# Kernel optimization log

Measured on AMD Instinct MI355X. Metric: run time of the kernel, lower is better.

## Reference

```python
import jax, jax.numpy as jnp
import numpy as np

T, B, D = 32, 16, 128


def _evolve(xr, xi, U):
    # xr, xi: [T,B,D,D]; U: [D,D,2] -> complex U x U^H per matrix
    Ur, Ui = U[..., 0], U[..., 1]
    r = jnp.einsum('ij,tbjk->tbik', Ur, xr) - jnp.einsum('ij,tbjk->tbik', Ui, xi)
    i = jnp.einsum('ij,tbjk->tbik', Ui, xr) + jnp.einsum('ij,tbjk->tbik', Ur, xi)
    out_r = jnp.einsum('tbik,jk->tbij', r, Ur) + jnp.einsum('tbik,jk->tbij', i, Ui)
    out_i = jnp.einsum('tbik,jk->tbij', i, Ur) - jnp.einsum('tbik,jk->tbij', r, Ui)
    return out_r, out_i


def _forward(inputs_real, inputs_imag, Uq, Uk, Uv):
    qr, qi = _evolve(inputs_real, inputs_imag, Uq)
    kr, ki = _evolve(inputs_real, inputs_imag, Uk)
    vr, vi = _evolve(inputs_real, inputs_imag, Uv)
    # trace(A @ B) = sum_ij A_ij * B_ji -> distance scores [Tq, Tk, B]
    tr_r = jnp.einsum('qbij,kbji->qkb', qr, kr) - jnp.einsum('qbij,kbji->qkb', qi, ki)
    tr_i = jnp.einsum('qbij,kbji->qkb', qr, ki) + jnp.einsum('qbij,kbji->qkb', qi, kr)
    dist = jnp.sqrt(tr_r * tr_r + tr_i * tr_i)
    # original builds scores via torch.tensor(list) -> values are detached
    dist = jax.lax.stop_gradient(dist)
    # original applies softmax over the LAST dim of the [Tk, B] score matrix,
    # i.e. over the batch dim (faithful reproduction)
    S = jax.nn.softmax(dist, axis=-1)  # [Tq, Tk, B]
    # original zip(values[0], values[1], scores) iterates the (real, imag)
    # components of the value at t=0 and t=1 against score rows 0 and 1
    s0 = S[:, 0, :, None, None]  # [Tq,B,1,1]
    s1 = S[:, 1, :, None, None]
    out_r = vr[0][None] * s0 + vi[0][None] * s1  # [Tq,B,D,D]
    out_i = vr[1][None] * s0 + vi[1][None] * s1
    return out_r, out_i


def setup_inputs() -> dict:
    key = jax.random.key(0)
    k0, k1, k2, k3, k4 = jax.random.split(key, 5)
    inputs_real = jax.random.normal(k0, (T, B, D, D), dtype=jnp.float32)
    inputs_imag = jax.random.normal(k1, (T, B, D, D), dtype=jnp.float32)
    eye = jnp.stack([jnp.eye(D, dtype=jnp.float32), jnp.zeros((D, D), jnp.float32)], axis=-1)
    Uq = eye + 0.05 * jax.random.normal(k2, (D, D, 2), dtype=jnp.float32)
    Uk = eye + 0.05 * jax.random.normal(k3, (D, D, 2), dtype=jnp.float32)
    Uv = eye + 0.05 * jax.random.normal(k4, (D, D, 2), dtype=jnp.float32)
    return {"inputs_real": inputs_real, "inputs_imag": inputs_imag, "Uq": Uq, "Uk": Uk, "Uv": Uv}


def reference(inputs_real, inputs_imag, Uq, Uk, Uv):
    return _forward(inputs_real, inputs_imag, Uq, Uk, Uv)
```

## Files before the change

kernel.cpp:

```cpp
#include <hip/hip_runtime.h>
#include <math.h>

#define TT 32
#define BB 16
#define DD 128
#define MAT 16384
#define OFF_MR   0
#define OFF_MI   16384
#define OFF_YTR  32768
#define OFF_YTI  (32768 + 64*16384)
#define OFF_ZSR  (OFF_YTI + 64*16384)
#define OFF_ZSI  (OFF_ZSR + 32*16384)
#define OFF_VR   (OFF_ZSI + 32*16384)
#define OFF_VI   (OFF_VR + 32*16384)
#define OFF_TR   (OFF_VI + 32*16384)
#define OFF_S    (OFF_TR + 2048)

__device__ __forceinline__ float dot4(float4 a, float4 b) {
    return a.x*b.x + a.y*b.y + a.z*b.z + a.w*b.w;
}

__global__ __launch_bounds__(128) void k_M(const float* __restrict__ Uq,
                                           const float* __restrict__ Uk,
                                           float* __restrict__ ws) {
    const int i = blockIdx.x;
    const int j = threadIdx.x;
    __shared__ float qr_s[128], qi_s[128];
    qr_s[j] = Uq[(j*128 + i)*2 + 0];
    qi_s[j] = Uq[(j*128 + i)*2 + 1];
    __syncthreads();
    const float2* Uk2 = (const float2*)Uk;
    float mr = 0.f, mi = 0.f;
    #pragma unroll 8
    for (int p = 0; p < 128; ++p) {
        float2 k2 = Uk2[p*128 + j];
        float qr = qr_s[p], qi = qi_s[p];
        mr += qr*k2.x + qi*k2.y;
        mi += qr*k2.y - qi*k2.x;
    }
    ws[OFF_MR + i*128 + j] = mr;
    ws[OFF_MI + i*128 + j] = mi;
}

template<int STAGE>
__global__ __launch_bounds__(256) void k_evolve(const float* __restrict__ xr,
                                                const float* __restrict__ xi,
                                                const float* __restrict__ Uv,
                                                float* __restrict__ ws) {
    const int bid = blockIdx.x;
    const int m   = bid >> 2;
    const int i0  = (bid & 3) * 32;
    const int tid = threadIdx.x;
    const int rp  = tid >> 4;
    const int jg  = tid & 15;

    __shared__ float Bt_r[16][128], Bt_i[16][128];
    __shared__ float At_r[32][17],  At_i[32][17];
    __shared__ float T_r[32][129],  T_i[32][129];

    float accr[2][8], acci[2][8];
    #pragma unroll
    for (int r = 0; r < 2; ++r)
        #pragma unroll
        for (int k = 0; k < 8; ++k) { accr[r][k] = 0.f; acci[r][k] = 0.f; }

    const float* Br;
    const float* Bi;
    if (STAGE == 0) { Br = xr + (m & 31) * MAT;      Bi = xi + (m & 31) * MAT; }
    else            { Br = ws + OFF_YTR + m * MAT;   Bi = ws + OFF_YTI + m * MAT; }

    for (int p0 = 0; p0 < 128; p0 += 16) {
        __syncthreads();
        #pragma unroll
        for (int w = 0; w < 2; ++w) {
            int l = w*256 + tid;
            int row = l >> 5, c4 = l & 31;
            ((float4*)Bt_r[row])[c4] = ((const float4*)Br)[(p0+row)*32 + c4];
            ((float4*)Bt_i[row])[c4] = ((const float4*)Bi)[(p0+row)*32 + c4];
        }
        #pragma unroll
        for (int w = 0; w < 2; ++w) {
            int l = w*256 + tid;
            int r = l >> 4, pp = l & 15;
            float ar, ai;
            if (m < 32) {
                ar = ws[OFF_MR + (i0+r)*128 + p0 + pp];
                ai = ws[OFF_MI + (i0+r)*128 + p0 + pp];
            } else {
                float2 u = ((const float2*)Uv)[(i0+r)*128 + p0 + pp];
                ar = u.x; ai = u.y;
            }
            At_r[r][pp] = ar; At_i[r][pp] = ai;
        }
        __syncthreads();
        #pragma unroll
        for (int pp = 0; pp < 16; ++pp) {
            const float ar0 = At_r[2*rp+0][pp], ai0 = At_i[2*rp+0][pp];
            const float ar1 = At_r[2*rp+1][pp], ai1 = At_i[2*rp+1][pp];
            const float4* br4 = (const float4*)(&Bt_r[pp][0]);
            const float4* bi4 = (const float4*)(&Bt_i[pp][0]);
#define CF(R, K, BR, BI)                                                        \
    do {                                                                        \
        const float aR_ = (R) ? ar1 : ar0; const float aI_ = (R) ? ai1 : ai0;   \
        if (STAGE == 0) { accr[R][K] += aR_*(BR) - aI_*(BI);                    \
                          acci[R][K] += aR_*(BI) + aI_*(BR); }                  \
        else            { accr[R][K] += aR_*(BR) + aI_*(BI);                    \
                          acci[R][K] += aR_*(BI) - aI_*(BR); }                  \
    } while (0)
            #pragma unroll
            for (int s = 0; s < 2; ++s) {
                const float4 brv = br4[jg + 16*s];
                const float4 biv = bi4[jg + 16*s];
                CF(0, s*4+0, brv.x, biv.x); CF(0, s*4+1, brv.y, biv.y);
                CF(0, s*4+2, brv.z, biv.z); CF(0, s*4+3, brv.w, biv.w);
                CF(1, s*4+0, brv.x, biv.x); CF(1, s*4+1, brv.y, biv.y);
                CF(1, s*4+2, brv.z, biv.z); CF(1, s*4+3, brv.w, biv.w);
            }
#undef CF
        }
    }

    const bool transpose_store = (STAGE == 0) || (m >= 32);
    if (transpose_store) {
        __syncthreads();
        #pragma unroll
        for (int r = 0; r < 2; ++r)
            #pragma unroll
            for (int s = 0; s < 2; ++s)
                #pragma unroll
                for (int q = 0; q < 4; ++q) {
                    T_r[2*rp+r][jg*4 + 64*s + q] = accr[r][s*4+q];
                    T_i[2*rp+r][jg*4 + 64*s + q] = acci[r][s*4+q];
                }
        __syncthreads();
        float* dstR; float* dstI;
        if (STAGE == 0) { dstR = ws + OFF_YTR + m*MAT;      dstI = ws + OFF_YTI + m*MAT; }
        else            { dstR = ws + OFF_VR + (m-32)*MAT;  dstI = ws + OFF_VI + (m-32)*MAT; }
        #pragma unroll
        for (int w = 0; w < 16; ++w) {
            int o = w*256 + tid;
            int c = o >> 5, ii = o & 31;
            dstR[c*128 + i0 + ii] = T_r[ii][c];
            dstI[c*128 + i0 + ii] = T_i[ii][c];
        }
    } else {
        float* dstR = ws + OFF_ZSR + m*MAT;
        float* dstI = ws + OFF_ZSI + m*MAT;
        #pragma unroll
        for (int r = 0; r < 2; ++r)
            #pragma unroll
            for (int s = 0; s < 2; ++s) {
                float4 vR = make_float4(accr[r][s*4+0], accr[r][s*4+1], accr[r][s*4+2], accr[r][s*4+3]);
                float4 vI = make_float4(acci[r][s*4+0], acci[r][s*4+1], acci[r][s*4+2], acci[r][s*4+3]);
                *(float4*)&dstR[(i0 + 2*rp + r)*128 + jg*4 + 64*s] = vR;
                *(float4*)&dstI[(i0 + 2*rp + r)*128 + jg*4 + 64*s] = vI;
            }
    }
}

__global__ __launch_bounds__(256) void k_trace(const float* __restrict__ xr,
                                               const float* __restrict__ xi,
                                               float* __restrict__ ws) {
    const int q = blockIdx.x >> 4, b = blockIdx.x & 15;
    const int tid = threadIdx.x;
    const float4* Xr4  = (const float4*)(xr + (q*16 + b)*MAT);
    const float4* Xi4  = (const float4*)(xi + (q*16 + b)*MAT);
    const float4* Z0r4 = (const float4*)(ws + OFF_ZSR + b*MAT);
    const float4* Z0i4 = (const float4*)(ws + OFF_ZSI + b*MAT);
    const float4* Z1r4 = (const float4*)(ws + OFF_ZSR + (16+b)*MAT);
    const float4* Z1i4 = (const float4*)(ws + OFF_ZSI + (16+b)*MAT);
    float r0 = 0.f, s0 = 0.f, r1 = 0.f, s1 = 0.f;
    #pragma unroll 4
    for (int w = 0; w < 16; ++w) {
        int e = w*256 + tid;
        float4 xrv = Xr4[e], xiv = Xi4[e];
        float4 z0r = Z0r4[e], z0i = Z0i4[e];
        float4 z1r = Z1r4[e], z1i = Z1i4[e];
        r0 += dot4(xrv, z0r) - dot4(xiv, z0i);
        s0 += dot4(xrv, z0i) + dot4(xiv, z0r);
        r1 += dot4(xrv, z1r) - dot4(xiv, z1i);
        s1 += dot4(xrv, z1i) + dot4(xiv, z1r);
    }
    #pragma unroll
    for (int off = 32; off > 0; off >>= 1) {
        r0 += __shfl_down(r0, off);
        s0 += __shfl_down(s0, off);
        r1 += __shfl_down(r1, off);
        s1 += __shfl_down(s1, off);
    }
    __shared__ float red[4][4];
    if ((tid & 63) == 0) {
        int wv = tid >> 6;
        red[wv][0] = r0; red[wv][1] = s0; red[wv][2] = r1; red[wv][3] = s1;
    }
    __syncthreads();
    if (tid == 0) {
        float a0 = red[0][0]+red[1][0]+red[2][0]+red[3][0];
        float a1 = red[0][1]+red[1][1]+red[2][1]+red[3][1];
        float a2 = red[0][2]+red[1][2]+red[2][2]+red[3][2];
        float a3 = red[0][3]+red[1][3]+red[2][3]+red[3][3];
        float* trp = ws + OFF_TR;
        trp[((q*2+0)*16 + b)*2 + 0] = a0;
        trp[((q*2+0)*16 + b)*2 + 1] = a1;
        trp[((q*2+1)*16 + b)*2 + 0] = a2;
        trp[((q*2+1)*16 + b)*2 + 1] = a3;
    }
}

__global__ __launch_bounds__(64) void k_softmax(float* __restrict__ ws) {
    const int t = threadIdx.x;
    const float* trp = ws + OFF_TR + t*32;
    float d[16];
    float mx = -1e30f;
    #pragma unroll
    for (int b = 0; b < 16; ++b) {
        float rr = trp[b*2+0], ii = trp[b*2+1];
        d[b] = sqrtf(rr*rr + ii*ii);
        mx = fmaxf(mx, d[b]);
    }
    float sum = 0.f;
    #pragma unroll
    for (int b = 0; b < 16; ++b) { d[b] = expf(d[b] - mx); sum += d[b]; }
    float inv = 1.f / sum;
    #pragma unroll
    for (int b = 0; b < 16; ++b) ws[OFF_S + t*16 + b] = d[b] * inv;
}

__global__ __launch_bounds__(256) void k_out(const float* __restrict__ ws,
                                             float* __restrict__ out) {
    const int t = blockIdx.x >> 4, b = blockIdx.x & 15;
    const float s0 = ws[OFF_S + (t*2+0)*16 + b];
    const float s1 = ws[OFF_S + (t*2+1)*16 + b];
    const float4* Vr0 = (const float4*)(ws + OFF_VR + b*MAT);
    const float4* Vi0 = (const float4*)(ws + OFF_VI + b*MAT);
    const float4* Vr1 = (const float4*)(ws + OFF_VR + (16+b)*MAT);
    const float4* Vi1 = (const float4*)(ws + OFF_VI + (16+b)*MAT);
    float4* outR = (float4*)out + (t*16 + b)*4096;
    float4* outI = (float4*)out + 2097152 + (t*16 + b)*4096;
    #pragma unroll 4
    for (int w = 0; w < 16; ++w) {
        int e = w*256 + threadIdx.x;
        float4 a = Vr0[e], bb = Vi0[e], c = Vr1[e], dd = Vi1[e];
        outR[e] = make_float4(a.x*s0 + bb.x*s1, a.y*s0 + bb.y*s1,
                              a.z*s0 + bb.z*s1, a.w*s0 + bb.w*s1);
        outI[e] = make_float4(c.x*s0 + dd.x*s1, c.y*s0 + dd.y*s1,
                              c.z*s0 + dd.z*s1, c.w*s0 + dd.w*s1);
    }
}

extern "C" void kernel_launch(void* const* d_in, const int* in_sizes, int n_in,
                              void* d_out, int out_size, void* d_ws, size_t ws_size,
                              hipStream_t stream) {
    const float* xr = (const float*)d_in[0];
    const float* xi = (const float*)d_in[1];
    const float* Uq = (const float*)d_in[2];
    const float* Uk = (const float*)d_in[3];
    const float* Uv = (const float*)d_in[4];
    float* ws  = (float*)d_ws;
    float* out = (float*)d_out;

    k_M<<<128, 128, 0, stream>>>(Uq, Uk, ws);
    k_evolve<0><<<256, 256, 0, stream>>>(xr, xi, Uv, ws);
    k_evolve<1><<<256, 256, 0, stream>>>(xr, xi, Uv, ws);
    k_trace<<<512, 256, 0, stream>>>(xr, xi, ws);
    k_softmax<<<1, 64, 0, stream>>>(ws);
    k_out<<<512, 256, 0, stream>>>(ws, out);
}
```

Baseline: 100.8 us.

## Double-buffer B tiles and retile evolve GEMM to 4x4 microtiles

Restructures the complex evolve GEMM kernel. The A operand is loaded in two 64-column halves, stored transposed and padded so each thread can fetch four rows with one float4. B tiles are software-pipelined by prefetching the next tile into registers while computing on the current shared-memory buffer. Each thread now computes a 4x4 complex micro-tile with contiguous column ownership instead of 2x8. The aim is fewer LDS loads per FMA and to hide global-load latency, at the cost of more registers and a shared-memory region that is reused for the transpose stage.

```diff
diff --git a/kernel.cpp b/kernel.cpp
--- a/kernel.cpp
+++ b/kernel.cpp
@@ -42,6 +42,7 @@
     ws[OFF_MI + i*128 + j] = mi;
 }
 
+#define AT_PAD 36
 template<int STAGE>
 __global__ __launch_bounds__(256) void k_evolve(const float* __restrict__ xr,
                                                 const float* __restrict__ xi,
@@ -51,87 +52,114 @@
     const int m   = bid >> 2;
     const int i0  = (bid & 3) * 32;
     const int tid = threadIdx.x;
-    const int rp  = tid >> 4;
-    const int jg  = tid & 15;
-
-    __shared__ float Bt_r[16][128], Bt_i[16][128];
-    __shared__ float At_r[32][17],  At_i[32][17];
-    __shared__ float T_r[32][129],  T_i[32][129];
-
-    float accr[2][8], acci[2][8];
-    #pragma unroll
-    for (int r = 0; r < 2; ++r)
-        #pragma unroll
-        for (int k = 0; k < 8; ++k) { accr[r][k] = 0.f; acci[r][k] = 0.f; }
+    const int rg  = tid >> 5;
+    const int cg  = tid & 31;
+
+    __shared__ __align__(16) float smem_f[2304*2 + 4096*2];
+    float* At_r = smem_f;
+    float* At_i = smem_f + 2304;
+    float* Bbuf = smem_f + 4608;
+    float* T_r = smem_f;
+    float* T_i = smem_f + 32*129;
+
+    float accr[4][4], acci[4][4];
+    #pragma unroll
+    for (int r = 0; r < 4; ++r)
+        #pragma unroll
+        for (int k = 0; k < 4; ++k) { accr[r][k] = 0.f; acci[r][k] = 0.f; }
 
     const float* Br;
     const float* Bi;
     if (STAGE == 0) { Br = xr + (m & 31) * MAT;      Bi = xi + (m & 31) * MAT; }
     else            { Br = ws + OFF_YTR + m * MAT;   Bi = ws + OFF_YTI + m * MAT; }
-
-    for (int p0 = 0; p0 < 128; p0 += 16) {
-        __syncthreads();
-        #pragma unroll
-        for (int w = 0; w < 2; ++w) {
-            int l = w*256 + tid;
-            int row = l >> 5, c4 = l & 31;
-            ((float4*)Bt_r[row])[c4] = ((const float4*)Br)[(p0+row)*32 + c4];
-            ((float4*)Bt_i[row])[c4] = ((const float4*)Bi)[(p0+row)*32 + c4];
-        }
-        #pragma unroll
-        for (int w = 0; w < 2; ++w) {
-            int l = w*256 + tid;
-            int r = l >> 4, pp = l & 15;
+    const float4* Br4 = (const float4*)Br;
+    const float4* Bi4 = (const float4*)Bi;
+
+    auto loadA = [&](int h) {
+        #pragma unroll
+        for (int w = 0; w < 8; ++w) {
+            int idx = w*256 + tid;
+            int r = idx >> 6;
+            int p = idx & 63;
             float ar, ai;
             if (m < 32) {
-                ar = ws[OFF_MR + (i0+r)*128 + p0 + pp];
-                ai = ws[OFF_MI + (i0+r)*128 + p0 + pp];
+                ar = ws[OFF_MR + (i0+r)*128 + h*64 + p];
+                ai = ws[OFF_MI + (i0+r)*128 + h*64 + p];
             } else {
-                float2 u = ((const float2*)Uv)[(i0+r)*128 + p0 + pp];
+                float2 u = ((const float2*)Uv)[(i0+r)*128 + h*64 + p];
                 ar = u.x; ai = u.y;
             }
-            At_r[r][pp] = ar; At_i[r][pp] = ai;
-        }
+            At_r[p*AT_PAD + r] = ar;
+            At_i[p*AT_PAD + r] = ai;
+        }
+    };
+
+    float4 pr0, pr1, pi0, pi1;
+    auto gloadB = [&](int t) {
+        int b0 = t*512;
+        pr0 = Br4[b0 + tid];
+        pr1 = Br4[b0 + 256 + tid];
+        pi0 = Bi4[b0 + tid];
+        pi1 = Bi4[b0 + 256 + tid];
+    };
+    auto writeB = [&](int buf) {
+        float4* dR = (float4*)(Bbuf + buf*4096);
+        float4* dI = (float4*)(Bbuf + buf*4096 + 2048);
+        dR[tid]       = pr0;
+        dR[tid + 256] = pr1;
+        dI[tid]       = pi0;
+        dI[tid + 256] = pi1;
+    };
+
+    loadA(0);
+    gloadB(0);
+    writeB(0);
+
+    for (int t = 0; t < 8; ++t) {
+        if (t < 7) gloadB(t+1);
         __syncthreads();
+        if (t == 4) { loadA(1); __syncthreads(); }
+        const float* bufR = Bbuf + (t&1)*4096;
+        const float* bufI = bufR + 2048;
         #pragma unroll
         for (int pp = 0; pp < 16; ++pp) {
-            const float ar0 = At_r[2*rp+0][pp], ai0 = At_i[2*rp+0][pp];
-            const float ar1 = At_r[2*rp+1][pp], ai1 = At_i[2*rp+1][pp];
-            const float4* br4 = (const float4*)(&Bt_r[pp][0]);
-            const float4* bi4 = (const float4*)(&Bt_i[pp][0]);
-#define CF(R, K, BR, BI)                                                        \
-    do {                                                                        \
-        const float aR_ = (R) ? ar1 : ar0; const float aI_ = (R) ? ai1 : ai0;   \
-        if (STAGE == 0) { accr[R][K] += aR_*(BR) - aI_*(BI);                    \
-                          acci[R][K] += aR_*(BI) + aI_*(BR); }                  \
-        else            { accr[R][K] += aR_*(BR) + aI_*(BI);                    \
-                          acci[R][K] += aR_*(BI) - aI_*(BR); }                  \
+            const int pl = ((t & 3) << 4) + pp;
+            const float4 ar4 = *(const float4*)&At_r[pl*AT_PAD + (rg<<2)];
+            const float4 ai4 = *(const float4*)&At_i[pl*AT_PAD + (rg<<2)];
+            const float4 brv = *(const float4*)&bufR[pp*128 + (cg<<2)];
+            const float4 biv = *(const float4*)&bufI[pp*128 + (cg<<2)];
+#define CROW(R, AR, AI)                                                          \
+    do {                                                                         \
+        const float aR_ = (AR), aI_ = (AI);                                      \
+        const float br_[4] = {brv.x, brv.y, brv.z, brv.w};                       \
+        const float bi_[4] = {biv.x, biv.y, biv.z, biv.w};                       \
+        _Pragma("unroll")                                                        \
+        for (int k = 0; k < 4; ++k) {                                            \
+            if (STAGE == 0) { accr[R][k] += aR_*br_[k] - aI_*bi_[k];             \
+                              acci[R][k] += aR_*bi_[k] + aI_*br_[k]; }           \
+            else            { accr[R][k] += aR_*br_[k] + aI_*bi_[k];             \
+                              acci[R][k] += aR_*bi_[k] - aI_*br_[k]; }           \
+        }                                                                        \
     } while (0)
-            #pragma unroll
-            for (int s = 0; s < 2; ++s) {
-                const float4 brv = br4[jg + 16*s];
-                const float4 biv = bi4[jg + 16*s];
-                CF(0, s*4+0, brv.x, biv.x); CF(0, s*4+1, brv.y, biv.y);
-                CF(0, s*4+2, brv.z, biv.z); CF(0, s*4+3, brv.w, biv.w);
-                CF(1, s*4+0, brv.x, biv.x); CF(1, s*4+1, brv.y, biv.y);
-                CF(1, s*4+2, brv.z, biv.z); CF(1, s*4+3, brv.w, biv.w);
-            }
-#undef CF
-        }
+            CROW(0, ar4.x, ai4.x);
+            CROW(1, ar4.y, ai4.y);
+            CROW(2, ar4.z, ai4.z);
+            CROW(3, ar4.w, ai4.w);
+#undef CROW
+        }
+        if (t < 7) writeB((t+1)&1);
     }
 
     const bool transpose_store = (STAGE == 0) || (m >= 32);
     if (transpose_store) {
         __syncthreads();
         #pragma unroll
-        for (int r = 0; r < 2; ++r)
+        for (int r = 0; r < 4; ++r)
             #pragma unroll
-            for (int s = 0; s < 2; ++s)
-                #pragma unroll
-                for (int q = 0; q < 4; ++q) {
-                    T_r[2*rp+r][jg*4 + 64*s + q] = accr[r][s*4+q];
-                    T_i[2*rp+r][jg*4 + 64*s + q] = acci[r][s*4+q];
-                }
+            for (int k = 0; k < 4; ++k) {
+                T_r[((rg<<2)+r)*129 + (cg<<2)+k] = accr[r][k];
+                T_i[((rg<<2)+r)*129 + (cg<<2)+k] = acci[r][k];
+            }
         __syncthreads();
         float* dstR; float* dstI;
         if (STAGE == 0) { dstR = ws + OFF_YTR + m*MAT;      dstI = ws + OFF_YTI + m*MAT; }
@@ -140,21 +168,19 @@
         for (int w = 0; w < 16; ++w) {
             int o = w*256 + tid;
             int c = o >> 5, ii = o & 31;
-            dstR[c*128 + i0 + ii] = T_r[ii][c];
-            dstI[c*128 + i0 + ii] = T_i[ii][c];
+            dstR[c*128 + i0 + ii] = T_r[ii*129 + c];
+            dstI[c*128 + i0 + ii] = T_i[ii*129 + c];
         }
     } else {
         float* dstR = ws + OFF_ZSR + m*MAT;
         float* dstI = ws + OFF_ZSI + m*MAT;
         #pragma unroll
-        for (int r = 0; r < 2; ++r)
-            #pragma unroll
-            for (int s = 0; s < 2; ++s) {
-                float4 vR = make_float4(accr[r][s*4+0], accr[r][s*4+1], accr[r][s*4+2], accr[r][s*4+3]);
-                float4 vI = make_float4(acci[r][s*4+0], acci[r][s*4+1], acci[r][s*4+2], acci[r][s*4+3]);
-                *(float4*)&dstR[(i0 + 2*rp + r)*128 + jg*4 + 64*s] = vR;
-                *(float4*)&dstI[(i0 + 2*rp + r)*128 + jg*4 + 64*s] = vI;
-            }
+        for (int r = 0; r < 4; ++r) {
+            float4 vR = make_float4(accr[r][0], accr[r][1], accr[r][2], accr[r][3]);
+            float4 vI = make_float4(acci[r][0], acci[r][1], acci[r][2], acci[r][3]);
+            *(float4*)&dstR[(i0 + (rg<<2) + r)*128 + (cg<<2)] = vR;
+            *(float4*)&dstI[(i0 + (rg<<2) + r)*128 + (cg<<2)] = vI;
+        }
     }
 }
 
```

Result: faster. 92.32 us (-8.4%).

## Fuse both evolve stages into one kernel keeping intermediate rows in shared memory

Applied to the files above, without the earlier changes.

Merges the two k_evolve launches into one k_fused kernel. Each block computes an 8-row strip of the first complex product, keeps it in shared memory, then multiplies it by the transposed second factor, which k_M now also precomputes. This removes the large Y intermediate written to and read back from global memory, and one launch. It also register-prefetches the next B tile during compute. The cost is smaller per-thread tiles (2x2 instead of 2x8), which means more blocks (1024) and lower arithmetic intensity per shared load. Each block also rereads full 128x128 B matrices for only 8 output rows.

```diff
diff --git a/kernel.cpp b/kernel.cpp
--- a/kernel.cpp
+++ b/kernel.cpp
@@ -1,15 +1,14 @@
 #include <hip/hip_runtime.h>
 #include <math.h>
 
-#define TT 32
-#define BB 16
-#define DD 128
 #define MAT 16384
 #define OFF_MR   0
 #define OFF_MI   16384
-#define OFF_YTR  32768
-#define OFF_YTI  (32768 + 64*16384)
-#define OFF_ZSR  (OFF_YTI + 64*16384)
+#define OFF_MTR  32768
+#define OFF_MTI  49152
+#define OFF_UVTR 65536
+#define OFF_UVTI 81920
+#define OFF_ZSR  2129920
 #define OFF_ZSI  (OFF_ZSR + 32*16384)
 #define OFF_VR   (OFF_ZSI + 32*16384)
 #define OFF_VI   (OFF_VR + 32*16384)
@@ -22,6 +21,7 @@
 
 __global__ __launch_bounds__(128) void k_M(const float* __restrict__ Uq,
                                            const float* __restrict__ Uk,
+                                           const float* __restrict__ Uv,
                                            float* __restrict__ ws) {
     const int i = blockIdx.x;
     const int j = threadIdx.x;
@@ -38,123 +38,162 @@
         mr += qr*k2.x + qi*k2.y;
         mi += qr*k2.y - qi*k2.x;
     }
-    ws[OFF_MR + i*128 + j] = mr;
-    ws[OFF_MI + i*128 + j] = mi;
-}
-
-template<int STAGE>
-__global__ __launch_bounds__(256) void k_evolve(const float* __restrict__ xr,
-                                                const float* __restrict__ xi,
-                                                const float* __restrict__ Uv,
-                                                float* __restrict__ ws) {
+    ws[OFF_MR  + i*128 + j] = mr;
+    ws[OFF_MI  + i*128 + j] = mi;
+    ws[OFF_MTR + j*128 + i] = mr;
+    ws[OFF_MTI + j*128 + i] = mi;
+    float2 uv = ((const float2*)Uv)[i*128 + j];
+    ws[OFF_UVTR + j*128 + i] = uv.x;
+    ws[OFF_UVTI + j*128 + i] = uv.y;
+}
+
+__global__ __launch_bounds__(256) void k_fused(const float* __restrict__ xr,
+                                               const float* __restrict__ xi,
+                                               const float* __restrict__ Uv,
+                                               float* __restrict__ ws) {
     const int bid = blockIdx.x;
-    const int m   = bid >> 2;
-    const int i0  = (bid & 3) * 32;
+    const int m   = bid & 63;
+    const int i0  = (bid >> 6) * 8;
     const int tid = threadIdx.x;
-    const int rp  = tid >> 4;
-    const int jg  = tid & 15;
-
-    __shared__ float Bt_r[16][128], Bt_i[16][128];
-    __shared__ float At_r[32][17],  At_i[32][17];
-    __shared__ float T_r[32][129],  T_i[32][129];
-
-    float accr[2][8], acci[2][8];
+    const int rp  = tid & 3;
+    const int cg  = tid >> 2;
+
+    __shared__ __align__(16) float smem_f[2048 + 4096];
+    float* At   = smem_f;
+    float* Bbuf = smem_f + 2048;
+
+    float accr[2][2], acci[2][2];
     #pragma unroll
     for (int r = 0; r < 2; ++r)
         #pragma unroll
-        for (int k = 0; k < 8; ++k) { accr[r][k] = 0.f; acci[r][k] = 0.f; }
-
-    const float* Br;
-    const float* Bi;
-    if (STAGE == 0) { Br = xr + (m & 31) * MAT;      Bi = xi + (m & 31) * MAT; }
-    else            { Br = ws + OFF_YTR + m * MAT;   Bi = ws + OFF_YTI + m * MAT; }
-
-    for (int p0 = 0; p0 < 128; p0 += 16) {
+        for (int k = 0; k < 2; ++k) { accr[r][k] = 0.f; acci[r][k] = 0.f; }
+
+    const float2* Uv2 = (const float2*)Uv;
+    const float4* Xr4 = (const float4*)(xr + (m & 31)*MAT);
+    const float4* Xi4 = (const float4*)(xi + (m & 31)*MAT);
+    const float4* P2r = (const float4*)(ws + (m < 32 ? OFF_MTR : OFF_UVTR));
+    const float4* P2i = (const float4*)(ws + (m < 32 ? OFF_MTI : OFF_UVTI));
+
+    #pragma unroll
+    for (int w = 0; w < 2; ++w) {
+        int slot = w*256 + tid;
+        int rs = slot & 3;
+        int p  = slot >> 2;
+        float ar0, ai0, ar1, ai1;
+        if (m < 32) {
+            ar0 = ws[OFF_MR + (i0 + rs*2    )*128 + p];
+            ai0 = ws[OFF_MI + (i0 + rs*2    )*128 + p];
+            ar1 = ws[OFF_MR + (i0 + rs*2 + 1)*128 + p];
+            ai1 = ws[OFF_MI + (i0 + rs*2 + 1)*128 + p];
+        } else {
+            float2 u0 = Uv2[(i0 + rs*2    )*128 + p];
+            float2 u1 = Uv2[(i0 + rs*2 + 1)*128 + p];
+            ar0 = u0.x; ai0 = u0.y; ar1 = u1.x; ai1 = u1.y;
+        }
+        *(float4*)&At[p*16 + rs*4] = make_float4(ar0, ai0, ar1, ai1);
+    }
+
+    float4 pr0, pr1, pi0, pi1;
+    auto gload = [&](const float4* R, const float4* I, int t) {
+        int b0 = t*512;
+        pr0 = R[b0 + tid];
+        pr1 = R[b0 + 256 + tid];
+        pi0 = I[b0 + tid];
+        pi1 = I[b0 + 256 + tid];
+    };
+    auto writeB = [&]() {
+        ((float4*)Bbuf)[tid]                = pr0;
+        ((float4*)Bbuf)[tid + 256]          = pr1;
+        ((float4*)(Bbuf + 2048))[tid]       = pi0;
+        ((float4*)(Bbuf + 2048))[tid + 256] = pi1;
+    };
+
+    gload(Xr4, Xi4, 0); writeB(); __syncthreads();
+    for (int t = 0; t < 8; ++t) {
+        if (t < 7) gload(Xr4, Xi4, t+1);
+        #pragma unroll
+        for (int pp = 0; pp < 16; ++pp) {
+            int p = (t<<4) + pp;
+            float4 a4  = *(const float4*)&At[p*16 + (rp<<2)];
+            float2 brv = *(const float2*)&Bbuf[pp*128 + (cg<<1)];
+            float2 biv = *(const float2*)&Bbuf[2048 + pp*128 + (cg<<1)];
+            accr[0][0] += a4.x*brv.x - a4.y*biv.x;
+            acci[0][0] += a4.x*biv.x + a4.y*brv.x;
+            accr[0][1] += a4.x*brv.y - a4.y*biv.y;
+            acci[0][1] += a4.x*biv.y + a4.y*brv.y;
+            accr[1][0] += a4.z*brv.x - a4.w*biv.x;
+            acci[1][0] += a4.z*biv.x + a4.w*brv.x;
+            accr[1][1] += a4.z*brv.y - a4.w*biv.y;
+            acci[1][1] += a4.z*biv.y + a4.w*brv.y;
+        }
         __syncthreads();
-        #pragma unroll
-        for (int w = 0; w < 2; ++w) {
-            int l = w*256 + tid;
-            int row = l >> 5, c4 = l & 31;
-            ((float4*)Bt_r[row])[c4] = ((const float4*)Br)[(p0+row)*32 + c4];
-            ((float4*)Bt_i[row])[c4] = ((const float4*)Bi)[(p0+row)*32 + c4];
-        }
-        #pragma unroll
-        for (int w = 0; w < 2; ++w) {
-            int l = w*256 + tid;
-            int r = l >> 4, pp = l & 15;
-            float ar, ai;
-            if (m < 32) {
-                ar = ws[OFF_MR + (i0+r)*128 + p0 + pp];
-                ai = ws[OFF_MI + (i0+r)*128 + p0 + pp];
-            } else {
-                float2 u = ((const float2*)Uv)[(i0+r)*128 + p0 + pp];
-                ar = u.x; ai = u.y;
-            }
-            At_r[r][pp] = ar; At_i[r][pp] = ai;
+        if (t < 7) { writeB(); __syncthreads(); }
+    }
+
+    gload(P2r, P2i, 0);
+    #pragma unroll
+    for (int k = 0; k < 2; ++k)
+        *(float4*)&At[((cg<<1)+k)*16 + (rp<<2)] =
+            make_float4(accr[0][k], acci[0][k], accr[1][k], acci[1][k]);
+    #pragma unroll
+    for (int r = 0; r < 2; ++r)
+        #pragma unroll
+        for (int k = 0; k < 2; ++k) { accr[r][k] = 0.f; acci[r][k] = 0.f; }
+    writeB();
+    __syncthreads();
+
+    for (int t = 0; t < 8; ++t) {
+        if (t < 7) gload(P2r, P2i, t+1);
+        #pragma unroll
+        for (int k2 = 0; k2 < 16; ++k2) {
+            int k = (t<<4) + k2;
+            float4 a4  = *(const float4*)&At[k*16 + (rp<<2)];
+            float2 urv = *(const float2*)&Bbuf[k2*128 + (cg<<1)];
+            float2 uiv = *(const float2*)&Bbuf[2048 + k2*128 + (cg<<1)];
+            accr[0][0] += a4.x*urv.x + a4.y*uiv.x;
+            acci[0][0] += a4.y*urv.x - a4.x*uiv.x;
+            accr[0][1] += a4.x*urv.y + a4.y*uiv.y;
+            acci[0][1] += a4.y*urv.y - a4.x*uiv.y;
+            accr[1][0] += a4.z*urv.x + a4.w*uiv.x;
+            acci[1][0] += a4.w*urv.x - a4.z*uiv.x;
+            accr[1][1] += a4.z*urv.y + a4.w*uiv.y;
+            acci[1][1] += a4.w*urv.y - a4.z*uiv.y;
         }
         __syncthreads();
-        #pragma unroll
-        for (int pp = 0; pp < 16; ++pp) {
-            const float ar0 = At_r[2*rp+0][pp], ai0 = At_i[2*rp+0][pp];
-            const float ar1 = At_r[2*rp+1][pp], ai1 = At_i[2*rp+1][pp];
-            const float4* br4 = (const float4*)(&Bt_r[pp][0]);
-            const float4* bi4 = (const float4*)(&Bt_i[pp][0]);
-#define CF(R, K, BR, BI)                                                        \
-    do {                                                                        \
-        const float aR_ = (R) ? ar1 : ar0; const float aI_ = (R) ? ai1 : ai0;   \
-        if (STAGE == 0) { accr[R][K] += aR_*(BR) - aI_*(BI);                    \
-                          acci[R][K] += aR_*(BI) + aI_*(BR); }                  \
-        else            { accr[R][K] += aR_*(BR) + aI_*(BI);                    \
-                          acci[R][K] += aR_*(BI) - aI_*(BR); }                  \
-    } while (0)
-            #pragma unroll
-            for (int s = 0; s < 2; ++s) {
-                const float4 brv = br4[jg + 16*s];
-                const float4 biv = bi4[jg + 16*s];
-                CF(0, s*4+0, brv.x, biv.x); CF(0, s*4+1, brv.y, biv.y);
-                CF(0, s*4+2, brv.z, biv.z); CF(0, s*4+3, brv.w, biv.w);
-                CF(1, s*4+0, brv.x, biv.x); CF(1, s*4+1, brv.y, biv.y);
-                CF(1, s*4+2, brv.z, biv.z); CF(1, s*4+3, brv.w, biv.w);
-            }
-#undef CF
-        }
-    }
-
-    const bool transpose_store = (STAGE == 0) || (m >= 32);
-    if (transpose_store) {
-        __syncthreads();
+        if (t < 7) { writeB(); __syncthreads(); }
+    }
+
+    if (m < 32) {
+        float* T_r = Bbuf;
+        float* T_i = Bbuf + 1056;
         #pragma unroll
         for (int r = 0; r < 2; ++r)
             #pragma unroll
-            for (int s = 0; s < 2; ++s)
-                #pragma unroll
-                for (int q = 0; q < 4; ++q) {
-                    T_r[2*rp+r][jg*4 + 64*s + q] = accr[r][s*4+q];
-                    T_i[2*rp+r][jg*4 + 64*s + q] = acci[r][s*4+q];
-                }
+            for (int k = 0; k < 2; ++k) {
+                T_r[((rp<<1)+r)*132 + (cg<<1)+k] = accr[r][k];
+                T_i[((rp<<1)+r)*132 + (cg<<1)+k] = acci[r][k];
+            }
         __syncthreads();
-        float* dstR; float* dstI;
-        if (STAGE == 0) { dstR = ws + OFF_YTR + m*MAT;      dstI = ws + OFF_YTI + m*MAT; }
-        else            { dstR = ws + OFF_VR + (m-32)*MAT;  dstI = ws + OFF_VI + (m-32)*MAT; }
-        #pragma unroll
-        for (int w = 0; w < 16; ++w) {
-            int o = w*256 + tid;
-            int c = o >> 5, ii = o & 31;
-            dstR[c*128 + i0 + ii] = T_r[ii][c];
-            dstI[c*128 + i0 + ii] = T_i[ii][c];
-        }
-    } else {
         float* dstR = ws + OFF_ZSR + m*MAT;
         float* dstI = ws + OFF_ZSI + m*MAT;
         #pragma unroll
-        for (int r = 0; r < 2; ++r)
-            #pragma unroll
-            for (int s = 0; s < 2; ++s) {
-                float4 vR = make_float4(accr[r][s*4+0], accr[r][s*4+1], accr[r][s*4+2], accr[r][s*4+3]);
-                float4 vI = make_float4(acci[r][s*4+0], acci[r][s*4+1], acci[r][s*4+2], acci[r][s*4+3]);
-                *(float4*)&dstR[(i0 + 2*rp + r)*128 + jg*4 + 64*s] = vR;
-                *(float4*)&dstI[(i0 + 2*rp + r)*128 + jg*4 + 64*s] = vI;
-            }
+        for (int w = 0; w < 4; ++w) {
+            int o  = w*256 + tid;
+            int c  = o >> 3;
+            int ii = o & 7;
+            dstR[c*128 + i0 + ii] = T_r[ii*132 + c];
+            dstI[c*128 + i0 + ii] = T_i[ii*132 + c];
+        }
+    } else {
+        float* dstR = ws + OFF_VR + (m-32)*MAT;
+        float* dstI = ws + OFF_VI + (m-32)*MAT;
+        #pragma unroll
+        for (int r = 0; r < 2; ++r) {
+            *(float2*)&dstR[(i0 + (rp<<1) + r)*128 + (cg<<1)] =
+                make_float2(accr[r][0], accr[r][1]);
+            *(float2*)&dstI[(i0 + (rp<<1) + r)*128 + (cg<<1)] =
+                make_float2(acci[r][0], acci[r][1]);
+        }
     }
 }
 
@@ -259,9 +298,8 @@
     float* ws  = (float*)d_ws;
     float* out = (float*)d_out;
 
-    k_M<<<128, 128, 0, stream>>>(Uq, Uk, ws);
-    k_evolve<0><<<256, 256, 0, stream>>>(xr, xi, Uv, ws);
-    k_evolve<1><<<256, 256, 0, stream>>>(xr, xi, Uv, ws);
+    k_M<<<128, 128, 0, stream>>>(Uq, Uk, Uv, ws);
+    k_fused<<<1024, 256, 0, stream>>>(xr, xi, Uv, ws);
     k_trace<<<512, 256, 0, stream>>>(xr, xi, ws);
     k_softmax<<<1, 64, 0, stream>>>(ws);
     k_out<<<512, 256, 0, stream>>>(ws, out);
```

Result: no change. 99.26 us (-1.5%).

## Fuse two evolve GEMM stages into one register-resident kernel using readlane broadcasts

Applied to the files above, without the earlier changes.

Replaces the two-kernel evolve (left multiply, write intermediate to workspace, then right multiply) with a single kernel. Each wave keeps its intermediate rows in registers and broadcasts them across lanes with readlane, so the large intermediate global buffer and one launch go away. k_M now also writes interleaved complex and transposed copies of M and Uv to make the loads coalesced. The new code has no shared-memory tiling and relies on scalar readlane broadcasts, which may limit throughput.

```diff
diff --git a/kernel.cpp b/kernel.cpp
--- a/kernel.cpp
+++ b/kernel.cpp
@@ -1,27 +1,26 @@
 #include <hip/hip_runtime.h>
 #include <math.h>
 
-#define TT 32
-#define BB 16
-#define DD 128
 #define MAT 16384
-#define OFF_MR   0
-#define OFF_MI   16384
-#define OFF_YTR  32768
-#define OFF_YTI  (32768 + 64*16384)
-#define OFF_ZSR  (OFF_YTI + 64*16384)
+#define OFF_MC   0
+#define OFF_MTC  32768
+#define OFF_UVTC 65536
+#define OFF_ZSR  2129920
 #define OFF_ZSI  (OFF_ZSR + 32*16384)
 #define OFF_VR   (OFF_ZSI + 32*16384)
 #define OFF_VI   (OFF_VR + 32*16384)
 #define OFF_TR   (OFF_VI + 32*16384)
 #define OFF_S    (OFF_TR + 2048)
 
+#define RLF(x, l) __int_as_float(__builtin_amdgcn_readlane(__float_as_int(x), (l)))
+
 __device__ __forceinline__ float dot4(float4 a, float4 b) {
     return a.x*b.x + a.y*b.y + a.z*b.z + a.w*b.w;
 }
 
 __global__ __launch_bounds__(128) void k_M(const float* __restrict__ Uq,
                                            const float* __restrict__ Uk,
+                                           const float* __restrict__ Uv,
                                            float* __restrict__ ws) {
     const int i = blockIdx.x;
     const int j = threadIdx.x;
@@ -38,124 +37,151 @@
         mr += qr*k2.x + qi*k2.y;
         mi += qr*k2.y - qi*k2.x;
     }
-    ws[OFF_MR + i*128 + j] = mr;
-    ws[OFF_MI + i*128 + j] = mi;
-}
-
-template<int STAGE>
-__global__ __launch_bounds__(256) void k_evolve(const float* __restrict__ xr,
-                                                const float* __restrict__ xi,
-                                                const float* __restrict__ Uv,
-                                                float* __restrict__ ws) {
+    ws[OFF_MC  + i*256 + 2*j]     = mr;
+    ws[OFF_MC  + i*256 + 2*j + 1] = mi;
+    ws[OFF_MTC + j*256 + 2*i]     = mr;
+    ws[OFF_MTC + j*256 + 2*i + 1] = mi;
+    float2 uv = ((const float2*)Uv)[i*128 + j];
+    ws[OFF_UVTC + j*256 + 2*i]     = uv.x;
+    ws[OFF_UVTC + j*256 + 2*i + 1] = uv.y;
+}
+
+__global__ __launch_bounds__(256) void k_fused(const float* __restrict__ xr,
+                                               const float* __restrict__ xi,
+                                               const float* __restrict__ Uv,
+                                               float* __restrict__ ws) {
     const int bid = blockIdx.x;
-    const int m   = bid >> 2;
-    const int i0  = (bid & 3) * 32;
+    const int m   = bid & 63;
+    const int i0  = (bid >> 6) * 16;
     const int tid = threadIdx.x;
-    const int rp  = tid >> 4;
-    const int jg  = tid & 15;
-
-    __shared__ float Bt_r[16][128], Bt_i[16][128];
-    __shared__ float At_r[32][17],  At_i[32][17];
-    __shared__ float T_r[32][129],  T_i[32][129];
-
-    float accr[2][8], acci[2][8];
-    #pragma unroll
-    for (int r = 0; r < 2; ++r)
+    const int wv  = tid >> 6;
+    const int L   = tid & 63;
+    const int r0  = i0 + wv*4;
+    const int cbase = 2*L;
+
+    __shared__ __align__(16) float T[2*16*132];
+
+    const float* Ap = (m < 32) ? (ws + OFF_MC) : Uv;
+    float a[16];
+    #pragma unroll
+    for (int r = 0; r < 4; ++r) {
+        float4 v = *(const float4*)&Ap[(r0 + r)*256 + 4*L];
+        a[r*2]     = v.x; a[r*2+1]   = v.y;
+        a[8+r*2]   = v.z; a[8+r*2+1] = v.w;
+    }
+
+    float y[16];
+    #pragma unroll
+    for (int g = 0; g < 16; ++g) y[g] = 0.f;
+
+    const float* Xr = xr + (m & 31)*MAT;
+    const float* Xi = xi + (m & 31)*MAT;
+
+    float2 Ar0, Ai0, Ar1, Ai1, Br0, Bi0, Br1, Bi1;
+#define LD1(PP, R0, I0, R1, I1) do { int _p = (PP);          \
+    R0 = *(const float2*)&Xr[_p*128 + cbase];                \
+    I0 = *(const float2*)&Xi[_p*128 + cbase];                \
+    R1 = *(const float2*)&Xr[(_p+1)*128 + cbase];            \
+    I1 = *(const float2*)&Xi[(_p+1)*128 + cbase]; } while(0)
+
+#define STEP1(IT, R0, I0, R1, I1) do {                       \
+    float s[16];                                             \
+    _Pragma("unroll")                                        \
+    for (int g = 0; g < 16; ++g) s[g] = RLF(a[g], (IT));     \
+    _Pragma("unroll")                                        \
+    for (int r = 0; r < 4; ++r) {                            \
+        float ar = s[r*2], ai = s[r*2+1];                    \
+        y[r*2]     += ar*R0.x - ai*I0.x;                     \
+        y[r*2+1]   += ar*I0.x + ai*R0.x;                     \
+        y[8+r*2]   += ar*R0.y - ai*I0.y;                     \
+        y[8+r*2+1] += ar*I0.y + ai*R0.y;                     \
+        float br = s[8+r*2], bi = s[8+r*2+1];                \
+        y[r*2]     += br*R1.x - bi*I1.x;                     \
+        y[r*2+1]   += br*I1.x + bi*R1.x;                     \
+        y[8+r*2]   += br*R1.y - bi*I1.y;                     \
+        y[8+r*2+1] += br*I1.y + bi*R1.y;                     \
+    } } while(0)
+
+    LD1(0, Ar0,Ai0,Ar1,Ai1);
+    LD1(2, Br0,Bi0,Br1,Bi1);
+    #pragma unroll 1
+    for (int it = 0; it < 64; it += 2) {
+        STEP1(it, Ar0,Ai0,Ar1,Ai1);
+        { int p = 2*it+4; if (p > 126) p = 126; LD1(p, Ar0,Ai0,Ar1,Ai1); }
+        STEP1(it+1, Br0,Bi0,Br1,Bi1);
+        { int p = 2*it+6; if (p > 126) p = 126; LD1(p, Br0,Bi0,Br1,Bi1); }
+    }
+
+    float z[16];
+    #pragma unroll
+    for (int g = 0; g < 16; ++g) z[g] = 0.f;
+    const float4* UT4 = (const float4*)(ws + (m < 32 ? OFF_MTC : OFF_UVTC));
+
+    float4 Ue, Uo, Ve, Vo;
+#define LD2(KK, E, O) do { int _k = (KK);                    \
+    E = UT4[_k*64 + L]; O = UT4[(_k+1)*64 + L]; } while(0)
+
+#define STEP2(IT, E, O) do {                                 \
+    float s[16];                                             \
+    _Pragma("unroll")                                        \
+    for (int g = 0; g < 16; ++g) s[g] = RLF(y[g], (IT));     \
+    _Pragma("unroll")                                        \
+    for (int r = 0; r < 4; ++r) {                            \
+        float yr = s[r*2], yi = s[r*2+1];                    \
+        z[r*2]     += yr*E.x + yi*E.y;                       \
+        z[r*2+1]   += yi*E.x - yr*E.y;                       \
+        z[8+r*2]   += yr*E.z + yi*E.w;                       \
+        z[8+r*2+1] += yi*E.z - yr*E.w;                       \
+        float wr = s[8+r*2], wi = s[8+r*2+1];                \
+        z[r*2]     += wr*O.x + wi*O.y;                       \
+        z[r*2+1]   += wi*O.x - wr*O.y;                       \
+        z[8+r*2]   += wr*O.z + wi*O.w;                       \
+        z[8+r*2+1] += wi*O.z - wr*O.w;                       \
+    } } while(0)
+
+    LD2(0, Ue, Uo);
+    LD2(2, Ve, Vo);
+    #pragma unroll 1
+    for (int it = 0; it < 64; it += 2) {
+        STEP2(it, Ue, Uo);
+        { int k = 2*it+4; if (k > 126) k = 126; LD2(k, Ue, Uo); }
+        STEP2(it+1, Ve, Vo);
+        { int k = 2*it+6; if (k > 126) k = 126; LD2(k, Ve, Vo); }
+    }
+
+    if (m < 32) {
+        float* T_r = T;
+        float* T_i = T + 16*132;
         #pragma unroll
-        for (int k = 0; k < 8; ++k) { accr[r][k] = 0.f; acci[r][k] = 0.f; }
-
-    const float* Br;
-    const float* Bi;
-    if (STAGE == 0) { Br = xr + (m & 31) * MAT;      Bi = xi + (m & 31) * MAT; }
-    else            { Br = ws + OFF_YTR + m * MAT;   Bi = ws + OFF_YTI + m * MAT; }
-
-    for (int p0 = 0; p0 < 128; p0 += 16) {
-        __syncthreads();
-        #pragma unroll
-        for (int w = 0; w < 2; ++w) {
-            int l = w*256 + tid;
-            int row = l >> 5, c4 = l & 31;
-            ((float4*)Bt_r[row])[c4] = ((const float4*)Br)[(p0+row)*32 + c4];
-            ((float4*)Bt_i[row])[c4] = ((const float4*)Bi)[(p0+row)*32 + c4];
-        }
-        #pragma unroll
-        for (int w = 0; w < 2; ++w) {
-            int l = w*256 + tid;
-            int r = l >> 4, pp = l & 15;
-            float ar, ai;
-            if (m < 32) {
-                ar = ws[OFF_MR + (i0+r)*128 + p0 + pp];
-                ai = ws[OFF_MI + (i0+r)*128 + p0 + pp];
-            } else {
-                float2 u = ((const float2*)Uv)[(i0+r)*128 + p0 + pp];
-                ar = u.x; ai = u.y;
-            }
-            At_r[r][pp] = ar; At_i[r][pp] = ai;
+        for (int r = 0; r < 4; ++r) {
+            int ii = wv*4 + r;
+            *(float2*)&T_r[ii*132 + cbase] = make_float2(z[r*2],   z[8+r*2]);
+            *(float2*)&T_i[ii*132 + cbase] = make_float2(z[r*2+1], z[8+r*2+1]);
         }
         __syncthreads();
-        #pragma unroll
-        for (int pp = 0; pp < 16; ++pp) {
-            const float ar0 = At_r[2*rp+0][pp], ai0 = At_i[2*rp+0][pp];
-            const float ar1 = At_r[2*rp+1][pp], ai1 = At_i[2*rp+1][pp];
-            const float4* br4 = (const float4*)(&Bt_r[pp][0]);
-            const float4* bi4 = (const float4*)(&Bt_i[pp][0]);
-#define CF(R, K, BR, BI)                                                        \
-    do {                                                                        \
-        const float aR_ = (R) ? ar1 : ar0; const float aI_ = (R) ? ai1 : ai0;   \
-        if (STAGE == 0) { accr[R][K] += aR_*(BR) - aI_*(BI);                    \
-                          acci[R][K] += aR_*(BI) + aI_*(BR); }                  \
-        else            { accr[R][K] += aR_*(BR) + aI_*(BI);                    \
-                          acci[R][K] += aR_*(BI) - aI_*(BR); }                  \
-    } while (0)
-            #pragma unroll
-            for (int s = 0; s < 2; ++s) {
-                const float4 brv = br4[jg + 16*s];
-                const float4 biv = bi4[jg + 16*s];
-                CF(0, s*4+0, brv.x, biv.x); CF(0, s*4+1, brv.y, biv.y);
-                CF(0, s*4+2, brv.z, biv.z); CF(0, s*4+3, brv.w, biv.w);
-                CF(1, s*4+0, brv.x, biv.x); CF(1, s*4+1, brv.y, biv.y);
-                CF(1, s*4+2, brv.z, biv.z); CF(1, s*4+3, brv.w, biv.w);
-            }
-#undef CF
-        }
-    }
-
-    const bool transpose_store = (STAGE == 0) || (m >= 32);
-    if (transpose_store) {
-        __syncthreads();
-        #pragma unroll
-        for (int r = 0; r < 2; ++r)
-            #pragma unroll
-            for (int s = 0; s < 2; ++s)
-                #pragma unroll
-                for (int q = 0; q < 4; ++q) {
-                    T_r[2*rp+r][jg*4 + 64*s + q] = accr[r][s*4+q];
-                    T_i[2*rp+r][jg*4 + 64*s + q] = acci[r][s*4+q];
-                }
-        __syncthreads();
-        float* dstR; float* dstI;
-        if (STAGE == 0) { dstR = ws + OFF_YTR + m*MAT;      dstI = ws + OFF_YTI + m*MAT; }
-        else            { dstR = ws + OFF_VR + (m-32)*MAT;  dstI = ws + OFF_VI + (m-32)*MAT; }
-        #pragma unroll
-        for (int w = 0; w < 16; ++w) {
-            int o = w*256 + tid;
-            int c = o >> 5, ii = o & 31;
-            dstR[c*128 + i0 + ii] = T_r[ii][c];
-            dstI[c*128 + i0 + ii] = T_i[ii][c];
-        }
-    } else {
         float* dstR = ws + OFF_ZSR + m*MAT;
         float* dstI = ws + OFF_ZSI + m*MAT;
         #pragma unroll
-        for (int r = 0; r < 2; ++r)
-            #pragma unroll
-            for (int s = 0; s < 2; ++s) {
-                float4 vR = make_float4(accr[r][s*4+0], accr[r][s*4+1], accr[r][s*4+2], accr[r][s*4+3]);
-                float4 vI = make_float4(acci[r][s*4+0], acci[r][s*4+1], acci[r][s*4+2], acci[r][s*4+3]);
-                *(float4*)&dstR[(i0 + 2*rp + r)*128 + jg*4 + 64*s] = vR;
-                *(float4*)&dstI[(i0 + 2*rp + r)*128 + jg*4 + 64*s] = vI;
-            }
-    }
+        for (int w = 0; w < 8; ++w) {
+            int o  = w*256 + tid;
+            int c  = o >> 4;
+            int ii = o & 15;
+            dstR[c*128 + i0 + ii] = T_r[ii*132 + c];
+            dstI[c*128 + i0 + ii] = T_i[ii*132 + c];
+        }
+    } else {
+        float* dstR = ws + OFF_VR + (m-32)*MAT;
+        float* dstI = ws + OFF_VI + (m-32)*MAT;
+        #pragma unroll
+        for (int r = 0; r < 4; ++r) {
+            *(float2*)&dstR[(r0 + r)*128 + cbase] = make_float2(z[r*2],   z[8+r*2]);
+            *(float2*)&dstI[(r0 + r)*128 + cbase] = make_float2(z[r*2+1], z[8+r*2+1]);
+        }
+    }
+#undef LD1
+#undef STEP1
+#undef LD2
+#undef STEP2
 }
 
 __global__ __launch_bounds__(256) void k_trace(const float* __restrict__ xr,
@@ -259,9 +285,8 @@
     float* ws  = (float*)d_ws;
     float* out = (float*)d_out;
 
-    k_M<<<128, 128, 0, stream>>>(Uq, Uk, ws);
-    k_evolve<0><<<256, 256, 0, stream>>>(xr, xi, Uv, ws);
-    k_evolve<1><<<256, 256, 0, stream>>>(xr, xi, Uv, ws);
+    k_M<<<128, 128, 0, stream>>>(Uq, Uk, Uv, ws);
+    k_fused<<<512, 256, 0, stream>>>(xr, xi, Uv, ws);
     k_trace<<<512, 256, 0, stream>>>(xr, xi, ws);
     k_softmax<<<1, 64, 0, stream>>>(ws);
     k_out<<<512, 256, 0, stream>>>(ws, out);
```

After: 120.6 us. +19.7%, slower.
